# Kernel optimization log

Hardware: AMD Instinct MI355X
Metric: run time of the kernel (lower is better)

Reference implementation:

```python
import jax, jax.numpy as jnp
import numpy as np

DIM = 768
NUM_HEADS = 12
HEAD_DIM = DIM // NUM_HEADS
SCALE = HEAD_DIM ** -0.5
B, N = 16, 640  # N = 8*8 + 24*24


def setup_inputs() -> dict:
    key = jax.random.key(0)
    ks = jax.random.split(key, 4)
    x = jax.random.normal(ks[0], (B, N, DIM), dtype=jnp.float32)
    # weights stored input-major: y = x @ W + b (equiv. to torch Linear with W = weight.T)
    qkv_w = jax.random.normal(ks[1], (DIM, 3 * DIM), dtype=jnp.float32) * (DIM ** -0.5)
    qkv_b = jnp.zeros((3 * DIM,), dtype=jnp.float32)
    proj_w = jax.random.normal(ks[2], (DIM, DIM), dtype=jnp.float32) * (DIM ** -0.5)
    proj_b = jnp.zeros((DIM,), dtype=jnp.float32)
    w = jnp.ones((2,), dtype=jnp.float32)
    return {"x": x, "qkv_w": qkv_w, "qkv_b": qkv_b, "proj_w": proj_w,
            "proj_b": proj_b, "w": w, "t_h": 8, "t_w": 8, "s_h": 24, "s_w": 24}


def reference(x, qkv_w, qkv_b, proj_w, proj_b, w, t_h, t_w, s_h, s_w):
    b, n, c = x.shape
    qkv = (x @ qkv_w + qkv_b).reshape(b, n, 3, NUM_HEADS, HEAD_DIM)
    qkv = jnp.transpose(qkv, (2, 0, 3, 1, 4))  # [3, B, H, N, D]
    q, k, v = qkv[0], qkv[1], qkv[2]
    attn = jnp.einsum('bhnd,bhmd->bhnm', q, k) * SCALE  # [B,H,N,N]
    attn0 = jax.nn.softmax(attn, axis=-1)
    attn1 = jnp.square(jax.nn.relu(attn))
    ws = jax.nn.softmax(w)  # exp(w_i)/sum(exp(w)) blend weights
    attn = attn0 * ws[0] + attn1 * ws[1]
    out = jnp.einsum('bhnm,bhmd->bhnd', attn, v)  # [B,H,N,D]
    out = jnp.transpose(out, (0, 2, 1, 3)).reshape(b, n, c)
    return out @ proj_w + proj_b
```

## Files before the change

kernel.cpp:

```cpp
#include <hip/hip_runtime.h>
#include <hip/hip_bf16.h>

typedef __attribute__((ext_vector_type(8))) short short8;
typedef __attribute__((ext_vector_type(4))) float floatx4;
typedef __hip_bfloat16 bf16;

#define DIM 768
#define NH 12
#define HD 64
#define BB 16
#define NN 640
#define BH (BB*NH)
#define MROWS (BB*NN)
#define QKVN (3*DIM)
#define QSCALE 0.18033688011113205f
#define LN2SQ 0.4804530139182014f

__device__ __forceinline__ floatx4 mfma16(short8 a, short8 b, floatx4 c) {
    return __builtin_amdgcn_mfma_f32_16x16x32_bf16(a, b, c, 0, 0, 0);
}

__device__ __forceinline__ void async_ld16(const bf16* g, bf16* l) {
    __builtin_amdgcn_global_load_lds(
        (const __attribute__((address_space(1))) void*)g,
        (__attribute__((address_space(3))) void*)l, 16, 0, 0);
}

__device__ __forceinline__ unsigned pack_trunc(float a, float b) {
    return __builtin_amdgcn_perm(__float_as_uint(b), __float_as_uint(a), 0x07060302u);
}

__device__ __forceinline__ float fexp2(float x) {
#if __has_builtin(__builtin_amdgcn_exp2f)
    return __builtin_amdgcn_exp2f(x);
#else
    return exp2f(x);
#endif
}


__global__ void cvt_x(const float* __restrict__ x, bf16* __restrict__ xb, int n4) {
    int i = blockIdx.x * blockDim.x + threadIdx.x;
    if (i >= n4) return;
    float4 v = ((const float4*)x)[i];
    bf16* p = xb + (size_t)i * 4;
    p[0] = __float2bfloat16(v.x);
    p[1] = __float2bfloat16(v.y);
    p[2] = __float2bfloat16(v.z);
    p[3] = __float2bfloat16(v.w);
}

__global__ void tr_cvt(const float* __restrict__ src, bf16* __restrict__ dst, int R, int C) {
    __shared__ float tile[32][33];
    int bx = blockIdx.x, by = blockIdx.y;
    int tx = threadIdx.x, ty = threadIdx.y;
    for (int j = 0; j < 4; ++j)
        tile[ty + j*8][tx] = src[(size_t)(by*32 + ty + j*8) * C + bx*32 + tx];
    __syncthreads();
    for (int j = 0; j < 4; ++j)
        dst[(size_t)(bx*32 + ty + j*8) * R + by*32 + tx] = __float2bfloat16(tile[tx][ty + j*8]);
}

template<int MODE>
__global__ __launch_bounds__(256) void gemm_bt(
    const bf16* __restrict__ A, const bf16* __restrict__ B, const float* __restrict__ bias,
    int M, int N, int K,
    bf16* __restrict__ outb, bf16* __restrict__ vTo, float* __restrict__ outf)
{
    __shared__ __align__(16) bf16 As[128*64];
    __shared__ __align__(16) bf16 Bs[128*64];

    const int t = threadIdx.x;
    const int lane = t & 63, wave = t >> 6;
    const int l15 = lane & 15, quad = lane >> 4;
    const int wm = (wave >> 1) * 64, wn = (wave & 1) * 64;
    const int m0 = blockIdx.y * 128, n0 = blockIdx.x * 128;

    floatx4 acc[4][4];
    floatx4 zero = {0.f, 0.f, 0.f, 0.f};
    for (int i = 0; i < 4; ++i)
        for (int j = 0; j < 4; ++j)
            acc[i][j] = zero;

    const int sw = l15 & 7;
    for (int kk = 0; kk < K; kk += 64) {
        __syncthreads();
        for (int s = 0; s < 4; ++s) {
            int cid = s * 256 + t;
            int row = cid >> 3;
            int gc  = ((t & 7) ^ (row & 7)) << 3;
            int lbase = (s * 256 + wave * 64) * 8;
            async_ld16(A + (size_t)(m0 + row) * K + kk + gc, As + lbase);
            async_ld16(B + (size_t)(n0 + row) * K + kk + gc, Bs + lbase);
        }
        __syncthreads();
        short8 af0[4], af1[4], bf0[4], bf1[4];
        for (int fm = 0; fm < 4; ++fm) {
            int base = (wm + fm*16 + l15) * 64 + ((quad ^ sw) << 3);
            af0[fm] = *(const short8*)(As + base);
            af1[fm] = *(const short8*)(As + (base ^ 32));
        }
        for (int fn = 0; fn < 4; ++fn) {
            int base = (wn + fn*16 + l15) * 64 + ((quad ^ sw) << 3);
            bf0[fn] = *(const short8*)(Bs + base);
            bf1[fn] = *(const short8*)(Bs + (base ^ 32));
        }
        for (int fm = 0; fm < 4; ++fm)
            for (int fn = 0; fn < 4; ++fn) {
                acc[fm][fn] = mfma16(af0[fm], bf0[fn], acc[fm][fn]);
                acc[fm][fn] = mfma16(af1[fm], bf1[fn], acc[fm][fn]);
            }
    }

    if (MODE == 0 && n0 >= 2*DIM) {
        __syncthreads();
        bf16* T4 = As + wave * 2048;
        const int bh   = (m0 / NN) * NH + ((n0 + wn) >> 6) - 24;
        const int tokb = (m0 % NN) + wm;
        for (int fn = 0; fn < 4; ++fn) {
            int n = n0 + wn + fn*16 + l15;
            float bn = bias[n];
            for (int fm = 0; fm < 4; ++fm) {
                float v0 = acc[fm][fn][0] + bn, v1 = acc[fm][fn][1] + bn;
                float v2 = acc[fm][fn][2] + bn, v3 = acc[fm][fn][3] + bn;
                *(uint2*)(T4 + fm*512 + l15*32 + quad*4) =
                    make_uint2(pack_trunc(v0, v1), pack_trunc(v2, v3));
            }
            uint4 r0 = *(const uint4*)(T4 + quad*512 + l15*32);
            uint4 r1 = *(const uint4*)(T4 + quad*512 + l15*32 + 8);
            int d = fn*16 + l15;
            bf16* dst = vTo + ((size_t)bh * HD + d) * NN + tokb + quad*16;
            *(uint4*)dst = r0;
            *(uint4*)(dst + 8) = r1;
        }
        return;
    }

    for (int fm = 0; fm < 4; ++fm) {
        for (int fn = 0; fn < 4; ++fn) {
            int n = n0 + wn + fn*16 + l15;
            float bn = bias[n];
            for (int r = 0; r < 4; ++r) {
                int m = m0 + wm + fm*16 + quad*4 + r;
                float v = acc[fm][fn][r] + bn;
                if (MODE == 0) {
                    if (n < DIM) v *= QSCALE;
                    outb[(size_t)m * N + n] = __float2bfloat16(v);
                } else {
                    outf[(size_t)m * N + n] = v;
                }
            }
        }
    }
}

__global__ __launch_bounds__(256) void attn_kernel(
    const bf16* __restrict__ qkv, const bf16* __restrict__ vT,
    const float* __restrict__ w2, bf16* __restrict__ ao)
{
    const int bh = blockIdx.x;
    const int b = bh / NH, h = bh - b * NH;
    const int t = threadIdx.x;
    const int wave = t >> 6, lane = t & 63;
    const int l15 = lane & 15, quad = lane >> 4;
    const int qrow0 = blockIdx.y * 64 + wave * 16;

    float w0 = w2[0], w1 = w2[1];
    float wmx = fmaxf(w0, w1);
    float e0 = __expf(w0 - wmx), e1 = __expf(w1 - wmx);
    float ws0 = e0 / (e0 + e1);
    float ws1 = (1.0f - ws0) * LN2SQ;

    __shared__ __align__(16) bf16 Kb[2][64*64];
    __shared__ __align__(16) bf16 Vb[2][64*64];
    __shared__ __align__(16) bf16 Ps[4][16*72];
    __shared__ __align__(16) bf16 Pr[4][16*72];

    const bf16* kb = qkv + (size_t)(b*NN)*QKVN + DIM + h*HD;
    const bf16* vb = vT + (size_t)bh * HD * NN;

    const bf16* qr = qkv + (size_t)(b*NN + qrow0 + l15) * QKVN + h*HD;
    short8 aq0 = *(const short8*)(qr + quad*8);
    short8 aq1 = *(const short8*)(qr + 32 + quad*8);

    const int srow = t >> 3;
    const int gc   = ((lane & 7) ^ (lane >> 3)) << 3;
    const bf16* kst = kb + (size_t)srow * QKVN + gc;
    const bf16* vst = vb + (size_t)srow * NN + gc;
    const int lb0 = (wave * 64) * 8;
    const int lb1 = (256 + wave * 64) * 8;

    async_ld16(kst,                     &Kb[0][lb0]);
    async_ld16(kst + (size_t)32 * QKVN, &Kb[0][lb1]);
    async_ld16(vst,                     &Vb[0][lb0]);
    async_ld16(vst + (size_t)32 * NN,   &Vb[0][lb1]);

    floatx4 zero = {0.f, 0.f, 0.f, 0.f};
    floatx4 accS[4], accR[4];
    for (int i = 0; i < 4; ++i) { accS[i] = zero; accR[i] = zero; }
    float lsum = 0.f;

    const int sw = l15 & 7;
    const int fbase = l15 * 64 + ((quad ^ sw) << 3);

    unsigned* PsW = (unsigned*)&Ps[wave][0];
    unsigned* PrW = (unsigned*)&Pr[wave][0];
    const int wb = l15*36 + quad*2;
    const bf16* PsR = &Ps[wave][l15*72 + quad*8];
    const bf16* PrR = &Pr[wave][l15*72 + quad*8];

#pragma unroll 2
    for (int kt = 0; kt < 10; ++kt) {
        const int cur = kt & 1;
        __syncthreads();
        if (kt + 1 < 10) {
            kst += (size_t)64 * QKVN;
            vst += 64;
            async_ld16(kst,                     &Kb[cur^1][lb0]);
            async_ld16(kst + (size_t)32 * QKVN, &Kb[cur^1][lb1]);
            async_ld16(vst,                     &Vb[cur^1][lb0]);
            async_ld16(vst + (size_t)32 * NN,   &Vb[cur^1][lb1]);
        }

        const bf16* Kc = &Kb[cur][0];
        const bf16* Vc = &Vb[cur][0];

        floatx4 s[4];
        for (int I = 0; I < 4; ++I) {
            short8 aklo = *(const short8*)(Kc + fbase + I*1024);
            short8 akhi = *(const short8*)(Kc + ((fbase + I*1024) ^ 32));
            s[I] = zero;
            s[I] = mfma16(aklo, aq0, s[I]);
            s[I] = mfma16(akhi, aq1, s[I]);
        }

        short8 bvlo[4], bvhi[4];
        for (int dt = 0; dt < 4; ++dt) {
            bvlo[dt] = *(const short8*)(Vc + fbase + dt*1024);
            bvhi[dt] = *(const short8*)(Vc + ((fbase + dt*1024) ^ 32));
        }

        for (int I = 0; I < 4; ++I) {
            float ex[4], rq[4];
            for (int r = 0; r < 4; ++r) {
                ex[r] = fexp2(s[I][r]);
                float m = fmaxf(s[I][r], 0.f);
                rq[r] = m * m;
                lsum += ex[r];
            }
            *(uint2*)(PsW + wb + I*8) = make_uint2(pack_trunc(ex[0],ex[1]), pack_trunc(ex[2],ex[3]));
            *(uint2*)(PrW + wb + I*8) = make_uint2(pack_trunc(rq[0],rq[1]), pack_trunc(rq[2],rq[3]));
        }

        short8 paSlo = *(const short8*)PsR;
        short8 paShi = *(const short8*)(PsR + 32);
        short8 paRlo = *(const short8*)PrR;
        short8 paRhi = *(const short8*)(PrR + 32);

        for (int dt = 0; dt < 4; ++dt) {
            accS[dt] = mfma16(paSlo, bvlo[dt], accS[dt]);
            accS[dt] = mfma16(paShi, bvhi[dt], accS[dt]);
            accR[dt] = mfma16(paRlo, bvlo[dt], accR[dt]);
            accR[dt] = mfma16(paRhi, bvhi[dt], accR[dt]);
        }
    }

    lsum += __shfl_xor(lsum, 16);
    lsum += __shfl_xor(lsum, 32);
    float invq[4];
    for (int r = 0; r < 4; ++r)
        invq[r] = 1.0f / __shfl(lsum, quad*4 + r);

    for (int dt = 0; dt < 4; ++dt) {
        for (int r = 0; r < 4; ++r) {
            float v = ws0 * accS[dt][r] * invq[r] + ws1 * accR[dt][r];
            int tok = qrow0 + quad*4 + r;
            ao[((size_t)(b * NN + tok)) * DIM + h * HD + dt*16 + l15] = __float2bfloat16(v);
        }
    }
}


extern "C" void kernel_launch(void* const* d_in, const int* in_sizes, int n_in,
                              void* d_out, int out_size, void* d_ws, size_t ws_size,
                              hipStream_t stream) {
    const float* x      = (const float*)d_in[0];
    const float* qkv_w  = (const float*)d_in[1];
    const float* qkv_b  = (const float*)d_in[2];
    const float* proj_w = (const float*)d_in[3];
    const float* proj_b = (const float*)d_in[4];
    const float* w2     = (const float*)d_in[5];
    float* out = (float*)d_out;

    bf16* xb   = (bf16*)d_ws;
    bf16* qwT  = xb   + (size_t)MROWS * DIM;
    bf16* pwT  = qwT  + (size_t)QKVN * DIM;
    bf16* qkvb = pwT  + (size_t)DIM * DIM;
    bf16* vT   = qkvb + (size_t)MROWS * QKVN;
    bf16* ao   = xb;

    cvt_x<<<(MROWS * DIM / 4 + 255) / 256, 256, 0, stream>>>(x, xb, MROWS * DIM / 4);
    tr_cvt<<<dim3(QKVN / 32, DIM / 32), dim3(32, 8), 0, stream>>>(qkv_w, qwT, DIM, QKVN);
    tr_cvt<<<dim3(DIM / 32, DIM / 32), dim3(32, 8), 0, stream>>>(proj_w, pwT, DIM, DIM);

    gemm_bt<0><<<dim3(QKVN / 128, MROWS / 128), 256, 0, stream>>>(
        xb, qwT, qkv_b, MROWS, QKVN, DIM, qkvb, vT, nullptr);

    attn_kernel<<<dim3(BH, NN / 64), 256, 0, stream>>>(qkvb, vT, w2, ao);

    gemm_bt<1><<<dim3(DIM / 128, MROWS / 128), 256, 0, stream>>>(
        ao, pwT, proj_b, MROWS, DIM, DIM, nullptr, nullptr, out);
}
```

Measured before the change: 225.1 us.

## Double-buffer GEMM LDS tiles and merge prep conversions into one kernel

The bf16 GEMM now uses two LDS buffers per operand and prefetches the next K-tile with async global-to-LDS loads while the current tile feeds the MFMAs. This removes one barrier per K step and hides load latency. In exchange, LDS use per block doubles, which can lower occupancy. The x conversion and the two weight transpose-conversions are also fused into a single launch to cut launch overhead.

```diff
diff --git a/kernel.cpp b/kernel.cpp
--- a/kernel.cpp
+++ b/kernel.cpp
@@ -16,6 +16,10 @@
 #define QSCALE 0.18033688011113205f
 #define LN2SQ 0.4804530139182014f
 
+#define CVT_BLK (MROWS*DIM/4/256)
+#define TRQ_BLK ((QKVN/32)*(DIM/32))
+#define TRP_BLK ((DIM/32)*(DIM/32))
+
 __device__ __forceinline__ floatx4 mfma16(short8 a, short8 b, floatx4 c) {
     return __builtin_amdgcn_mfma_f32_16x16x32_bf16(a, b, c, 0, 0, 0);
 }
@@ -38,22 +42,40 @@
 #endif
 }
 
-
-__global__ void cvt_x(const float* __restrict__ x, bf16* __restrict__ xb, int n4) {
-    int i = blockIdx.x * blockDim.x + threadIdx.x;
-    if (i >= n4) return;
-    float4 v = ((const float4*)x)[i];
-    bf16* p = xb + (size_t)i * 4;
-    p[0] = __float2bfloat16(v.x);
-    p[1] = __float2bfloat16(v.y);
-    p[2] = __float2bfloat16(v.z);
-    p[3] = __float2bfloat16(v.w);
-}
-
-__global__ void tr_cvt(const float* __restrict__ src, bf16* __restrict__ dst, int R, int C) {
+__global__ void prep_all(const float* __restrict__ x,
+                         const float* __restrict__ qkv_w,
+                         const float* __restrict__ proj_w,
+                         bf16* __restrict__ xb,
+                         bf16* __restrict__ qwT,
+                         bf16* __restrict__ pwT)
+{
     __shared__ float tile[32][33];
-    int bx = blockIdx.x, by = blockIdx.y;
-    int tx = threadIdx.x, ty = threadIdx.y;
+    const int id = blockIdx.x;
+    const int t = threadIdx.x;
+
+    if (id < CVT_BLK) {
+        int i = id * 256 + t;
+        float4 v = ((const float4*)x)[i];
+        bf16* p = xb + (size_t)i * 4;
+        p[0] = __float2bfloat16(v.x);
+        p[1] = __float2bfloat16(v.y);
+        p[2] = __float2bfloat16(v.z);
+        p[3] = __float2bfloat16(v.w);
+        return;
+    }
+
+    const float* src; bf16* dst; int C, bx, by;
+    if (id < CVT_BLK + TRQ_BLK) {
+        int j = id - CVT_BLK;
+        bx = j % (QKVN/32); by = j / (QKVN/32);
+        src = qkv_w; dst = qwT; C = QKVN;
+    } else {
+        int j = id - CVT_BLK - TRQ_BLK;
+        bx = j % (DIM/32); by = j / (DIM/32);
+        src = proj_w; dst = pwT; C = DIM;
+    }
+    const int R = DIM;
+    const int tx = t & 31, ty = t >> 5;
     for (int j = 0; j < 4; ++j)
         tile[ty + j*8][tx] = src[(size_t)(by*32 + ty + j*8) * C + bx*32 + tx];
     __syncthreads();
@@ -67,8 +89,8 @@
     int M, int N, int K,
     bf16* __restrict__ outb, bf16* __restrict__ vTo, float* __restrict__ outf)
 {
-    __shared__ __align__(16) bf16 As[128*64];
-    __shared__ __align__(16) bf16 Bs[128*64];
+    __shared__ __align__(16) bf16 As[2][128*64];
+    __shared__ __align__(16) bf16 Bs[2][128*64];
 
     const int t = threadIdx.x;
     const int lane = t & 63, wave = t >> 6;
@@ -82,28 +104,40 @@
         for (int j = 0; j < 4; ++j)
             acc[i][j] = zero;
 
+    const int trow = t >> 3;
+    const int gc = ((t & 7) ^ (trow & 7)) << 3;
+    const bf16* aA = A + (size_t)(m0 + trow) * K + gc;
+    const bf16* aB = B + (size_t)(n0 + trow) * K + gc;
+    const int lb = wave * 512;
+
+    for (int s = 0; s < 4; ++s) {
+        async_ld16(aA + (size_t)s*32*K, &As[0][s*2048 + lb]);
+        async_ld16(aB + (size_t)s*32*K, &Bs[0][s*2048 + lb]);
+    }
+
     const int sw = l15 & 7;
-    for (int kk = 0; kk < K; kk += 64) {
+    const int nit = K >> 6;
+    for (int kt = 0; kt < nit; ++kt) {
+        const int cur = kt & 1;
         __syncthreads();
-        for (int s = 0; s < 4; ++s) {
-            int cid = s * 256 + t;
-            int row = cid >> 3;
-            int gc  = ((t & 7) ^ (row & 7)) << 3;
-            int lbase = (s * 256 + wave * 64) * 8;
-            async_ld16(A + (size_t)(m0 + row) * K + kk + gc, As + lbase);
-            async_ld16(B + (size_t)(n0 + row) * K + kk + gc, Bs + lbase);
-        }
-        __syncthreads();
+        if (kt + 1 < nit) {
+            const bf16* pA = aA + (size_t)(kt+1)*64;
+            const bf16* pB = aB + (size_t)(kt+1)*64;
+            for (int s = 0; s < 4; ++s) {
+                async_ld16(pA + (size_t)s*32*K, &As[cur^1][s*2048 + lb]);
+                async_ld16(pB + (size_t)s*32*K, &Bs[cur^1][s*2048 + lb]);
+            }
+        }
         short8 af0[4], af1[4], bf0[4], bf1[4];
         for (int fm = 0; fm < 4; ++fm) {
             int base = (wm + fm*16 + l15) * 64 + ((quad ^ sw) << 3);
-            af0[fm] = *(const short8*)(As + base);
-            af1[fm] = *(const short8*)(As + (base ^ 32));
+            af0[fm] = *(const short8*)(&As[cur][base]);
+            af1[fm] = *(const short8*)(&As[cur][base ^ 32]);
         }
         for (int fn = 0; fn < 4; ++fn) {
             int base = (wn + fn*16 + l15) * 64 + ((quad ^ sw) << 3);
-            bf0[fn] = *(const short8*)(Bs + base);
-            bf1[fn] = *(const short8*)(Bs + (base ^ 32));
+            bf0[fn] = *(const short8*)(&Bs[cur][base]);
+            bf1[fn] = *(const short8*)(&Bs[cur][base ^ 32]);
         }
         for (int fm = 0; fm < 4; ++fm)
             for (int fn = 0; fn < 4; ++fn) {
@@ -113,8 +147,7 @@
     }
 
     if (MODE == 0 && n0 >= 2*DIM) {
-        __syncthreads();
-        bf16* T4 = As + wave * 2048;
+        bf16* T4 = &As[0][0] + wave * 2048;
         const int bh   = (m0 / NN) * NH + ((n0 + wn) >> 6) - 24;
         const int tokb = (m0 % NN) + wm;
         for (int fn = 0; fn < 4; ++fn) {
@@ -299,9 +332,8 @@
     bf16* vT   = qkvb + (size_t)MROWS * QKVN;
     bf16* ao   = xb;
 
-    cvt_x<<<(MROWS * DIM / 4 + 255) / 256, 256, 0, stream>>>(x, xb, MROWS * DIM / 4);
-    tr_cvt<<<dim3(QKVN / 32, DIM / 32), dim3(32, 8), 0, stream>>>(qkv_w, qwT, DIM, QKVN);
-    tr_cvt<<<dim3(DIM / 32, DIM / 32), dim3(32, 8), 0, stream>>>(proj_w, pwT, DIM, DIM);
+    prep_all<<<CVT_BLK + TRQ_BLK + TRP_BLK, 256, 0, stream>>>(
+        x, qkv_w, proj_w, xb, qwT, pwT);
 
     gemm_bt<0><<<dim3(QKVN / 128, MROWS / 128), 256, 0, stream>>>(
         xb, qwT, qkv_b, MROWS, QKVN, DIM, qkvb, vT, nullptr);
```

Result: faster. 217.1 us (-3.6%).
